# Optimization experiments

Measured on AMD Instinct MI355X. Metric: run time of the kernel, lower is better.

Reference implementation:

```python
import jax, jax.numpy as jnp
import numpy as np

EMBED_DIM = 1024
NUM_HEADS = 16
HEAD_DIM = EMBED_DIM // NUM_HEADS
SCALE = HEAD_DIM ** -0.5


def setup_inputs() -> dict:
    key = jax.random.key(0)
    k1, k2, k3, k4 = jax.random.split(key, 4)
    B, N, D = 2, 2048, EMBED_DIM
    x = jax.random.normal(k1, (B, N, D), dtype=jnp.float32)
    # nn.Linear weights stored as [out, in]; we keep [in, out] for x @ W
    w_qkv = jax.random.normal(k2, (D, 3 * D), dtype=jnp.float32) * (D ** -0.5)
    w_proj = jax.random.normal(k3, (D, D), dtype=jnp.float32) * (D ** -0.5)
    b_proj = jax.random.normal(k4, (D,), dtype=jnp.float32) * 0.01
    return {"x": x, "w_qkv": w_qkv, "w_proj": w_proj, "b_proj": b_proj}


def reference(x, w_qkv, w_proj, b_proj):
    B, N, D = x.shape
    H, Hd = NUM_HEADS, HEAD_DIM
    qkv = x @ w_qkv  # [B, N, 3D]
    q, k, v = jnp.split(qkv, 3, axis=-1)
    # [B, N, D] -> [B, H, N, Hd]
    split_heads = lambda t: t.reshape(B, N, H, Hd).transpose(0, 2, 1, 3)
    q, k, v = split_heads(q), split_heads(k), split_heads(v)
    a = jnp.einsum("bhqd,bhkd->bhqk", q, k) * SCALE
    a = jax.nn.softmax(a, axis=-1)
    out = jnp.einsum("bhqk,bhkd->bhqd", a, v)
    out = out.transpose(0, 2, 1, 3).reshape(B, N, D)
    return out @ w_proj + b_proj
```

## Files before the change

### kernel.cpp

```cpp
#include <hip/hip_runtime.h>
#include <stdint.h>

typedef __attribute__((ext_vector_type(8))) short bf16x8;
typedef __attribute__((ext_vector_type(4))) float f32x4;
typedef __attribute__((ext_vector_type(4))) float float4v;
typedef __attribute__((ext_vector_type(8))) unsigned short u16x8;

#define DEV __device__ __forceinline__

DEV unsigned short f2bf(float f) {
    union { float f; uint32_t u; } v; v.f = f;
    uint32_t u = v.u;
    return (unsigned short)((u + 0x7FFFu + ((u >> 16) & 1u)) >> 16);
}

DEV unsigned int cvt_pk_bf16(float lo, float hi) {
    unsigned int r;
    asm("v_cvt_pk_bf16_f32 %0, %1, %2" : "=v"(r) : "v"(lo), "v"(hi));
    return r;
}

#if __has_builtin(__builtin_amdgcn_global_load_lds)
#define HAVE_GLDS 1
typedef const unsigned char __attribute__((address_space(1)))* as1p;
typedef unsigned char __attribute__((address_space(3)))* as3p;
DEV void gload16(const unsigned short* g, unsigned short* l) {
    __builtin_amdgcn_global_load_lds((as1p)(const void*)g, (as3p)(void*)l, 16, 0, 0);
}
#else
#define HAVE_GLDS 0
#endif

__global__ void k_cvt_all(const float* __restrict__ x, unsigned short* __restrict__ xb,
                          const float* __restrict__ wqkv, unsigned short* __restrict__ wqkvT,
                          const float* __restrict__ wproj, unsigned short* __restrict__ wprojT) {
    __shared__ alignas(16) unsigned short tile[64][65];
    const int blk = blockIdx.x;
    const int t = threadIdx.x;
    if (blk < 4096) {
        const int i = blk * 256 + t;
        float4v v = *(const float4v*)(x + (size_t)i * 4);
        union { unsigned short s[4]; uint64_t q; } o;
        o.s[0] = f2bf(v[0]); o.s[1] = f2bf(v[1]); o.s[2] = f2bf(v[2]); o.s[3] = f2bf(v[3]);
        *(uint64_t*)(xb + (size_t)i * 4) = o.q;
        return;
    }
    const float* w; unsigned short* wt; int R, C, bx, by;
    if (blk < 4864) {
        const int b2 = blk - 4096;
        w = wqkv; wt = wqkvT; R = 1024; C = 3072;
        bx = b2 % 48; by = b2 / 48;
    } else {
        const int b3 = blk - 4864;
        w = wproj; wt = wprojT; R = 1024; C = 1024;
        bx = b3 % 16; by = b3 / 16;
    }
    const int tr = by * 64, tc = bx * 64;
#pragma unroll
    for (int p = 0; p < 4; ++p) {
        int r = p * 16 + (t >> 4);
        int c = (t & 15) * 4;
        float4v v = *(const float4v*)(w + (size_t)(tr + r) * C + tc + c);
#pragma unroll
        for (int j = 0; j < 4; ++j) tile[r][c + j] = f2bf(v[j]);
    }
    __syncthreads();
#pragma unroll
    for (int p = 0; p < 2; ++p) {
        int r2 = p * 32 + (t >> 3);
        int k0 = (t & 7) * 8;
        u16x8 o;
#pragma unroll
        for (int j = 0; j < 8; ++j) o[j] = tile[k0 + j][r2];
        *(u16x8*)(wt + (size_t)(tc + r2) * R + tr + k0) = o;
    }
}

template <int OUT_BF16, int BM, int BN, int NTY>
__global__ __launch_bounds__(256)
void k_gemm_bt(const unsigned short* __restrict__ A,
               const unsigned short* __restrict__ Bt,
               void* __restrict__ Cp, const float* __restrict__ bias,
               unsigned short* __restrict__ vt_out,
               int M, int N, int K) {
    constexpr int MFR = BM / 32;
    constexpr int NFR = BN / 32;
    __shared__ alignas(16) unsigned short lA[BM * 64];
    __shared__ alignas(16) unsigned short lB[BN * 64];
    const int t = threadIdx.x;
    const int w = t >> 6, l = t & 63;
    const int l15 = l & 15, l4 = l >> 4;
    const int wm = (w >> 1) * (BM / 2), wn = (w & 1) * (BN / 2);

    const int cpx = gridDim.x >> 3;
    const int wk = (blockIdx.x & 7) * cpx + (blockIdx.x >> 3);
    const int bx = wk / NTY, by = wk % NTY;
    const size_t bm = (size_t)by * BM, bn = (size_t)bx * BN;

    int offA[MFR][2], offB[NFR][2];
#pragma unroll
    for (int f = 0; f < MFR; ++f) {
        const int ra = wm + f * 16 + l15;
#pragma unroll
        for (int kc = 0; kc < 2; ++kc)
            offA[f][kc] = ra * 64 + (((kc * 4 + l4) ^ (ra & 7)) << 3);
    }
#pragma unroll
    for (int f = 0; f < NFR; ++f) {
        const int rb = wn + f * 16 + l15;
#pragma unroll
        for (int kc = 0; kc < 2; ++kc)
            offB[f][kc] = rb * 64 + (((kc * 4 + l4) ^ (rb & 7)) << 3);
    }

#if HAVE_GLDS
    const int srow8 = l >> 3;
    const int scol  = (l & 7) ^ srow8;
    const unsigned short* gA = A  + (bm + w * (BM / 4) + srow8) * (size_t)K + scol * 8;
    const unsigned short* gB = Bt + (bn + w * (BN / 4) + srow8) * (size_t)K + scol * 8;
    unsigned short* dA = lA + (w * (BM / 4)) * 64;
    unsigned short* dB = lB + (w * (BN / 4)) * 64;
#else
    const int srow = t >> 3, sslot = t & 7;
    const int swoff = srow * 64 + ((sslot ^ (srow & 7)) << 3);
    const unsigned short* pA = A + (bm + srow) * (size_t)K + sslot * 8;
    const unsigned short* pB = Bt + (bn + srow) * (size_t)K + sslot * 8;
#endif

    const f32x4 zf = {0.f, 0.f, 0.f, 0.f};
    f32x4 acc[MFR][NFR];
#pragma unroll
    for (int i = 0; i < MFR; ++i)
#pragma unroll
        for (int j = 0; j < NFR; ++j) acc[i][j] = zf;

    for (int kt = 0; kt < K; kt += 64) {
#if HAVE_GLDS
        __syncthreads();
#pragma unroll
        for (int i = 0; i < BM / 32; ++i)
            gload16(gA + (size_t)i * 8 * K + kt, dA + i * 8 * 64);
#pragma unroll
        for (int i = 0; i < BN / 32; ++i)
            gload16(gB + (size_t)i * 8 * K + kt, dB + i * 8 * 64);
        __syncthreads();
#else
        bf16x8 ra[BM / 32], rb[BN / 32];
#pragma unroll
        for (int p = 0; p < BM / 32; ++p)
            ra[p] = *(const bf16x8*)(pA + (size_t)p * 32 * K + kt);
#pragma unroll
        for (int p = 0; p < BN / 32; ++p)
            rb[p] = *(const bf16x8*)(pB + (size_t)p * 32 * K + kt);
        __syncthreads();
#pragma unroll
        for (int p = 0; p < BM / 32; ++p)
            *(bf16x8*)(lA + p * 32 * 64 + swoff) = ra[p];
#pragma unroll
        for (int p = 0; p < BN / 32; ++p)
            *(bf16x8*)(lB + p * 32 * 64 + swoff) = rb[p];
        __syncthreads();
#endif
#pragma unroll
        for (int kc = 0; kc < 2; ++kc) {
            bf16x8 af[MFR], bfr[NFR];
#pragma unroll
            for (int f = 0; f < MFR; ++f) af[f] = *(const bf16x8*)(lA + offA[f][kc]);
#pragma unroll
            for (int f = 0; f < NFR; ++f) bfr[f] = *(const bf16x8*)(lB + offB[f][kc]);
#pragma unroll
            for (int mf = 0; mf < MFR; ++mf)
#pragma unroll
                for (int nf = 0; nf < NFR; ++nf)
                    acc[mf][nf] = __builtin_amdgcn_mfma_f32_16x16x32_bf16(
                        af[mf], bfr[nf], acc[mf][nf], 0, 0, 0);
        }
    }

    if (OUT_BF16) {
        if (vt_out && bn >= 2048) {
            const int bb = (int)(bm >> 11);
            const int n0 = (int)(bm & 2047) + wm + l4 * 4;
#pragma unroll
            for (int nf = 0; nf < NFR; ++nf) {
                const int d = (int)(bn - 2048) + wn + nf * 16 + l15;
                unsigned short* vrow = vt_out + ((size_t)(bb * 16 + (d >> 6)) * 64 + (d & 63)) * 2048;
#pragma unroll
                for (int mf = 0; mf < MFR; ++mf) {
                    union { unsigned short s[4]; uint64_t q; } u;
#pragma unroll
                    for (int j = 0; j < 4; ++j) u.s[j] = f2bf(acc[mf][nf][j]);
                    *(uint64_t*)(vrow + n0 + mf * 16) = u.q;
                }
            }
        } else {
            unsigned short* C = (unsigned short*)Cp;
#pragma unroll
            for (int mf = 0; mf < MFR; ++mf)
#pragma unroll
                for (int nf = 0; nf < NFR; ++nf) {
                    const size_t row = bm + wm + mf * 16 + l4 * 4;
                    const size_t col = bn + wn + nf * 16 + l15;
#pragma unroll
                    for (int j = 0; j < 4; ++j)
                        C[(row + j) * (size_t)N + col] = f2bf(acc[mf][nf][j]);
                }
        }
    } else {
        float* C = (float*)Cp;
#pragma unroll
        for (int nf = 0; nf < NFR; ++nf) {
            const size_t col = bn + wn + nf * 16 + l15;
            const float bv = bias[col];
#pragma unroll
            for (int mf = 0; mf < MFR; ++mf) {
                const size_t row = bm + wm + mf * 16 + l4 * 4;
#pragma unroll
                for (int j = 0; j < 4; ++j)
                    C[(row + j) * (size_t)N + col] = acc[mf][nf][j] + bv;
            }
        }
    }
}

__global__ __launch_bounds__(256, 4)
void k_attn(const unsigned short* __restrict__ qkv, const unsigned short* __restrict__ vt,
            unsigned short* __restrict__ attn_out) {
    __shared__ alignas(16) unsigned short lK[2][64 * 64];
    __shared__ alignas(16) unsigned short lV[2][64 * 64];
    __shared__ alignas(16) unsigned short lP[4][16 * 64];
    const int t = threadIdx.x, w = t >> 6, l = t & 63;
    const int l15 = l & 15, l4 = l >> 4;
    const int wk = (blockIdx.x & 7) * 128 + (blockIdx.x >> 3);
    const int bh = wk >> 5, b = bh >> 4, h = bh & 15;
    const int qb = (wk & 31) * 64;
    const float QSCALE = 0.18033688011112042f;

    const unsigned short* qptr =
        qkv + (size_t)(b * 2048 + qb + w * 16 + l15) * 3072 + h * 64 + l4 * 8;
    const bf16x8 aq0 = *(const bf16x8*)(qptr);
    const bf16x8 aq1 = *(const bf16x8*)(qptr + 32);

    const int srow = t >> 3, sslot = t & 7;
    const int swoff = srow * 64 + ((sslot ^ (srow & 7)) << 3);
    const unsigned short* kptr = qkv + (size_t)(b * 2048 + srow) * 3072 + 1024 + h * 64 + sslot * 8;
    const unsigned short* vptr = vt + (size_t)(bh * 64 + srow) * 2048 + sslot * 8;

    int offK[4][2];
#pragma unroll
    for (int nf = 0; nf < 4; ++nf) {
        const int r = nf * 16 + l15;
#pragma unroll
        for (int kc = 0; kc < 2; ++kc)
            offK[nf][kc] = r * 64 + (((kc * 4 + l4) ^ (r & 7)) << 3);
    }
    int offPw[4];
#pragma unroll
    for (int nf = 0; nf < 4; ++nf) {
        const int c = nf * 16 + l4 * 4;
        offPw[nf] = l15 * 64 + (((c >> 3) ^ (l15 & 7)) << 3) + (c & 7);
    }

    const f32x4 zf = {0.f, 0.f, 0.f, 0.f};
    f32x4 o[4];
#pragma unroll
    for (int df = 0; df < 4; ++df) o[df] = zf;
    f32x4 accl = zf;
    float m_run = -1e30f;
    unsigned short* Pw = &lP[w][0];
    const bf16x8 ones8 = {(short)0x3F80, (short)0x3F80, (short)0x3F80, (short)0x3F80,
                          (short)0x3F80, (short)0x3F80, (short)0x3F80, (short)0x3F80};

    {
        bf16x8 rk[2], rv[2];
#pragma unroll
        for (int p = 0; p < 2; ++p) {
            rk[p] = *(const bf16x8*)(kptr + (size_t)(p * 32) * 3072);
            rv[p] = *(const bf16x8*)(vptr + (size_t)(p * 32) * 2048);
        }
#pragma unroll
        for (int p = 0; p < 2; ++p) {
            *(bf16x8*)(&lK[0][0] + p * 32 * 64 + swoff) = rk[p];
            *(bf16x8*)(&lV[0][0] + p * 32 * 64 + swoff) = rv[p];
        }
        __syncthreads();
    }

#pragma unroll 2
    for (int kt = 0; kt < 2048; kt += 64) {
        const int cur = (kt >> 6) & 1;
        const unsigned short* K = &lK[cur][0];
        const unsigned short* V = &lV[cur][0];

        bf16x8 rk[2], rv[2];
        const bool more = (kt + 64) < 2048;
        if (more) {
#pragma unroll
            for (int p = 0; p < 2; ++p) {
                rk[p] = *(const bf16x8*)(kptr + (size_t)(kt + 64 + p * 32) * 3072);
                rv[p] = *(const bf16x8*)(vptr + (size_t)(p * 32) * 2048 + kt + 64);
            }
        }

        f32x4 s[4];
        __builtin_amdgcn_s_setprio(1);
#pragma unroll
        for (int nf = 0; nf < 4; ++nf) {
            const bf16x8 kf0 = *(const bf16x8*)(K + offK[nf][0]);
            const bf16x8 kf1 = *(const bf16x8*)(K + offK[nf][1]);
            f32x4 a = zf;
            a = __builtin_amdgcn_mfma_f32_16x16x32_bf16(kf0, aq0, a, 0, 0, 0);
            a = __builtin_amdgcn_mfma_f32_16x16x32_bf16(kf1, aq1, a, 0, 0, 0);
            s[nf] = a;
        }
        __builtin_amdgcn_s_setprio(0);

        float mx = fmaxf(fmaxf(s[0][0], s[0][1]), s[0][2]);
        mx = fmaxf(fmaxf(mx, s[0][3]), s[1][0]);
        mx = fmaxf(fmaxf(mx, s[1][1]), s[1][2]);
        mx = fmaxf(fmaxf(mx, s[1][3]), s[2][0]);
        mx = fmaxf(fmaxf(mx, s[2][1]), s[2][2]);
        mx = fmaxf(fmaxf(mx, s[2][3]), s[3][0]);
        mx = fmaxf(fmaxf(mx, s[3][1]), s[3][2]);
        mx = fmaxf(mx, s[3][3]);
        mx = fmaxf(mx, __shfl_xor(mx, 16));
        mx = fmaxf(mx, __shfl_xor(mx, 32));
        mx *= QSCALE;

        if (!__all(mx <= m_run + 8.0f)) {
            const float mn = fmaxf(m_run, mx);
            const float alpha = exp2f(m_run - mn);
            m_run = mn;
            const float a0 = __shfl(alpha, l4 * 4 + 0);
            const float a1 = __shfl(alpha, l4 * 4 + 1);
            const float a2 = __shfl(alpha, l4 * 4 + 2);
            const float a3 = __shfl(alpha, l4 * 4 + 3);
#pragma unroll
            for (int df = 0; df < 4; ++df) {
                o[df][0] *= a0; o[df][1] *= a1; o[df][2] *= a2; o[df][3] *= a3;
            }
            accl[0] *= a0; accl[1] *= a1; accl[2] *= a2; accl[3] *= a3;
        }

#pragma unroll
        for (int nf = 0; nf < 4; ++nf) {
            const float p0 = exp2f(fmaf(s[nf][0], QSCALE, -m_run));
            const float p1 = exp2f(fmaf(s[nf][1], QSCALE, -m_run));
            const float p2 = exp2f(fmaf(s[nf][2], QSCALE, -m_run));
            const float p3 = exp2f(fmaf(s[nf][3], QSCALE, -m_run));
            union { unsigned int d[2]; uint64_t q; } u;
            u.d[0] = cvt_pk_bf16(p0, p1);
            u.d[1] = cvt_pk_bf16(p2, p3);
            *(uint64_t*)(Pw + offPw[nf]) = u.q;
        }

        const bf16x8 ap0 = *(const bf16x8*)(Pw + l15 * 64 + ((l4 ^ (l15 & 7)) << 3));
        const bf16x8 ap1 = *(const bf16x8*)(Pw + l15 * 64 + (((4 + l4) ^ (l15 & 7)) << 3));
        __builtin_amdgcn_s_setprio(1);
        accl = __builtin_amdgcn_mfma_f32_16x16x32_bf16(ap0, ones8, accl, 0, 0, 0);
        accl = __builtin_amdgcn_mfma_f32_16x16x32_bf16(ap1, ones8, accl, 0, 0, 0);
#pragma unroll
        for (int df = 0; df < 4; ++df) {
            const int r = df * 16 + l15;
            const bf16x8 bv0 = *(const bf16x8*)(V + r * 64 + ((l4 ^ (r & 7)) << 3));
            const bf16x8 bv1 = *(const bf16x8*)(V + r * 64 + (((4 + l4) ^ (r & 7)) << 3));
            o[df] = __builtin_amdgcn_mfma_f32_16x16x32_bf16(ap0, bv0, o[df], 0, 0, 0);
            o[df] = __builtin_amdgcn_mfma_f32_16x16x32_bf16(ap1, bv1, o[df], 0, 0, 0);
        }
        __builtin_amdgcn_s_setprio(0);

        if (more) {
#pragma unroll
            for (int p = 0; p < 2; ++p) {
                *(bf16x8*)(&lK[cur ^ 1][0] + p * 32 * 64 + swoff) = rk[p];
                *(bf16x8*)(&lV[cur ^ 1][0] + p * 32 * 64 + swoff) = rv[p];
            }
        }
        __syncthreads();
    }

    const float r0 = 1.0f / accl[0];
    const float r1 = 1.0f / accl[1];
    const float r2 = 1.0f / accl[2];
    const float r3 = 1.0f / accl[3];
    const int rowb = b * 2048 + qb + w * 16 + l4 * 4;
#pragma unroll
    for (int df = 0; df < 4; ++df) {
        const int d = df * 16 + l15;
        attn_out[(size_t)(rowb + 0) * 1024 + h * 64 + d] = f2bf(o[df][0] * r0);
        attn_out[(size_t)(rowb + 1) * 1024 + h * 64 + d] = f2bf(o[df][1] * r1);
        attn_out[(size_t)(rowb + 2) * 1024 + h * 64 + d] = f2bf(o[df][2] * r2);
        attn_out[(size_t)(rowb + 3) * 1024 + h * 64 + d] = f2bf(o[df][3] * r3);
    }
}

extern "C" void kernel_launch(void* const* d_in, const int* in_sizes, int n_in,
                              void* d_out, int out_size, void* d_ws, size_t ws_size,
                              hipStream_t stream) {
    const float* x      = (const float*)d_in[0];
    const float* w_qkv  = (const float*)d_in[1];
    const float* w_proj = (const float*)d_in[2];
    const float* b_proj = (const float*)d_in[3];
    float* out = (float*)d_out;

    char* ws = (char*)d_ws;
    unsigned short* xb     = (unsigned short*)(ws + 0);
    unsigned short* wqkvT  = (unsigned short*)(ws + 8388608);
    unsigned short* wprojT = (unsigned short*)(ws + 14680064);
    unsigned short* qkv    = (unsigned short*)(ws + 16777216);
    unsigned short* vt     = (unsigned short*)(ws + 41943040);
    unsigned short* attn   = (unsigned short*)(ws + 50331648);

    k_cvt_all<<<dim3(5120), dim3(256), 0, stream>>>(x, xb, w_qkv, wqkvT, w_proj, wprojT);
    k_gemm_bt<1, 128, 128, 32><<<dim3(768), dim3(256), 0, stream>>>(
        xb, wqkvT, (void*)qkv, (const float*)nullptr, vt, 4096, 3072, 1024);
    k_attn<<<dim3(1024), dim3(256), 0, stream>>>(qkv, vt, attn);
    k_gemm_bt<0, 64, 64, 64><<<dim3(1024), dim3(256), 0, stream>>>(
        attn, wprojT, (void*)out, b_proj, (unsigned short*)nullptr, 4096, 1024, 1024);
}
```

Before: 128.2 us.

## Use direct global-to-LDS loads for attention K/V and retile QKV GEMM

The attention kernel now streams K and V tiles straight from global memory into LDS with global_load_lds, where before it loaded them into registers and then stored them to LDS. The XOR swizzle is moved onto the global source address so the LDS layout stays the same. The QKV GEMM tile changes from 128x128 to 128x96, giving 1024 blocks instead of 768. Its epilogue now chooses per fragment between writing the transposed V buffer and the plain output, because a 96-wide tile can straddle the V boundary. The intent is to cut VGPR pressure and LDS store instructions in attention and to spread the GEMM over more blocks.

```diff
diff --git a/kernel.cpp b/kernel.cpp
--- a/kernel.cpp
+++ b/kernel.cpp
@@ -178,12 +178,14 @@
     }
 
     if (OUT_BF16) {
-        if (vt_out && bn >= 2048) {
-            const int bb = (int)(bm >> 11);
-            const int n0 = (int)(bm & 2047) + wm + l4 * 4;
-#pragma unroll
-            for (int nf = 0; nf < NFR; ++nf) {
-                const int d = (int)(bn - 2048) + wn + nf * 16 + l15;
+        unsigned short* C = (unsigned short*)Cp;
+#pragma unroll
+        for (int nf = 0; nf < NFR; ++nf) {
+            const int col0 = (int)bn + wn + nf * 16;
+            if (vt_out && col0 >= 2048) {
+                const int bb = (int)(bm >> 11);
+                const int n0 = (int)(bm & 2047) + wm + l4 * 4;
+                const int d = col0 - 2048 + l15;
                 unsigned short* vrow = vt_out + ((size_t)(bb * 16 + (d >> 6)) * 64 + (d & 63)) * 2048;
 #pragma unroll
                 for (int mf = 0; mf < MFR; ++mf) {
@@ -192,19 +194,16 @@
                     for (int j = 0; j < 4; ++j) u.s[j] = f2bf(acc[mf][nf][j]);
                     *(uint64_t*)(vrow + n0 + mf * 16) = u.q;
                 }
-            }
-        } else {
-            unsigned short* C = (unsigned short*)Cp;
-#pragma unroll
-            for (int mf = 0; mf < MFR; ++mf)
-#pragma unroll
-                for (int nf = 0; nf < NFR; ++nf) {
+            } else {
+                const size_t col = (size_t)col0 + l15;
+#pragma unroll
+                for (int mf = 0; mf < MFR; ++mf) {
                     const size_t row = bm + wm + mf * 16 + l4 * 4;
-                    const size_t col = bn + wn + nf * 16 + l15;
 #pragma unroll
                     for (int j = 0; j < 4; ++j)
                         C[(row + j) * (size_t)N + col] = f2bf(acc[mf][nf][j]);
                 }
+            }
         }
     } else {
         float* C = (float*)Cp;
@@ -241,10 +240,17 @@
     const bf16x8 aq0 = *(const bf16x8*)(qptr);
     const bf16x8 aq1 = *(const bf16x8*)(qptr + 32);
 
+#if HAVE_GLDS
+    const int gr = l >> 3;
+    const int gs = (l & 7) ^ gr;
+    const unsigned short* gK = qkv + (size_t)(b * 2048 + w * 16 + gr) * 3072 + 1024 + h * 64 + gs * 8;
+    const unsigned short* gV = vt + (size_t)(bh * 64 + w * 16 + gr) * 2048 + gs * 8;
+#else
     const int srow = t >> 3, sslot = t & 7;
     const int swoff = srow * 64 + ((sslot ^ (srow & 7)) << 3);
     const unsigned short* kptr = qkv + (size_t)(b * 2048 + srow) * 3072 + 1024 + h * 64 + sslot * 8;
     const unsigned short* vptr = vt + (size_t)(bh * 64 + srow) * 2048 + sslot * 8;
+#endif
 
     int offK[4][2];
 #pragma unroll
@@ -271,6 +277,14 @@
     const bf16x8 ones8 = {(short)0x3F80, (short)0x3F80, (short)0x3F80, (short)0x3F80,
                           (short)0x3F80, (short)0x3F80, (short)0x3F80, (short)0x3F80};
 
+#if HAVE_GLDS
+#pragma unroll
+    for (int i = 0; i < 2; ++i) {
+        gload16(gK + (size_t)i * 8 * 3072, &lK[0][(w * 16 + i * 8) * 64]);
+        gload16(gV + (size_t)i * 8 * 2048, &lV[0][(w * 16 + i * 8) * 64]);
+    }
+    __syncthreads();
+#else
     {
         bf16x8 rk[2], rv[2];
 #pragma unroll
@@ -285,15 +299,25 @@
         }
         __syncthreads();
     }
+#endif
 
 #pragma unroll 2
     for (int kt = 0; kt < 2048; kt += 64) {
         const int cur = (kt >> 6) & 1;
         const unsigned short* K = &lK[cur][0];
         const unsigned short* V = &lV[cur][0];
-
+        const bool more = (kt + 64) < 2048;
+
+#if HAVE_GLDS
+        if (more) {
+#pragma unroll
+            for (int i = 0; i < 2; ++i) {
+                gload16(gK + (size_t)(kt + 64 + i * 8) * 3072, &lK[cur ^ 1][(w * 16 + i * 8) * 64]);
+                gload16(gV + (size_t)i * 8 * 2048 + kt + 64,   &lV[cur ^ 1][(w * 16 + i * 8) * 64]);
+            }
+        }
+#else
         bf16x8 rk[2], rv[2];
-        const bool more = (kt + 64) < 2048;
         if (more) {
 #pragma unroll
             for (int p = 0; p < 2; ++p) {
@@ -301,6 +325,7 @@
                 rv[p] = *(const bf16x8*)(vptr + (size_t)(p * 32) * 2048 + kt + 64);
             }
         }
+#endif
 
         f32x4 s[4];
         __builtin_amdgcn_s_setprio(1);
@@ -369,6 +394,7 @@
         }
         __builtin_amdgcn_s_setprio(0);
 
+#if !HAVE_GLDS
         if (more) {
 #pragma unroll
             for (int p = 0; p < 2; ++p) {
@@ -376,6 +402,7 @@
                 *(bf16x8*)(&lV[cur ^ 1][0] + p * 32 * 64 + swoff) = rv[p];
             }
         }
+#endif
         __syncthreads();
     }
 
@@ -412,7 +439,7 @@
     unsigned short* attn   = (unsigned short*)(ws + 50331648);
 
     k_cvt_all<<<dim3(5120), dim3(256), 0, stream>>>(x, xb, w_qkv, wqkvT, w_proj, wprojT);
-    k_gemm_bt<1, 128, 128, 32><<<dim3(768), dim3(256), 0, stream>>>(
+    k_gemm_bt<1, 128, 96, 32><<<dim3(1024), dim3(256), 0, stream>>>(
         xb, wqkvT, (void*)qkv, (const float*)nullptr, vt, 4096, 3072, 1024);
     k_attn<<<dim3(1024), dim3(256), 0, stream>>>(qkv, vt, attn);
     k_gemm_bt<0, 64, 64, 64><<<dim3(1024), dim3(256), 0, stream>>>(
```

New measurement: 131.3 us. 1.02x slower.
